# Kernel optimization log

Measured on AMD Instinct MI355X. Metric: run time of the kernel, lower is better.

The kernel has to match this reference:

```python
import jax, jax.numpy as jnp
import numpy as np

B, T, C, COND, H = 64, 4096, 64, 512, 256
SCALE_EPS = 1e-6
LOGSCALE_FACTOR = 3.0  # glow LinearZeros convention
LEAK = 0.01            # torch LeakyReLU default slope


def setup_inputs() -> dict:
    key = jax.random.key(0)
    ks = jax.random.split(key, 10)
    perm = jnp.asarray(np.random.RandomState(0).permutation(C), dtype=jnp.int32)
    return {
        "input_seq": jax.random.normal(ks[0], (B, T, C), jnp.float32),
        "speech_cond": jax.random.normal(ks[1], (B, T, COND), jnp.float32),
        "actnorm_bias": 0.1 * jax.random.normal(ks[2], (C,), jnp.float32),
        "actnorm_logs": 0.1 * jax.random.normal(ks[3], (C,), jnp.float32),
        "perm": perm,
        "W1": jax.random.normal(ks[4], (C // 2 + COND, H), jnp.float32) / np.sqrt(C // 2 + COND),
        "b1": 0.01 * jax.random.normal(ks[5], (H,), jnp.float32),
        "W2": 0.05 * jax.random.normal(ks[6], (H, C), jnp.float32) / np.sqrt(H),
        "b2": 0.01 * jax.random.normal(ks[7], (C,), jnp.float32),
        "logs2": 0.05 * jax.random.normal(ks[8], (C,), jnp.float32),
    }


def reference(input_seq, speech_cond, actnorm_bias, actnorm_logs, perm, W1, b1, W2, b2, logs2):
    # The torch module loops over timesteps, but each step is independent
    # (no RNN state is used), so we batch all timesteps at once.
    # --- ActNorm2d (per-channel affine); pixels=1 per timestep ---
    z = (input_seq + actnorm_bias) * jnp.exp(actnorm_logs)          # [B,T,C]
    logdet = jnp.full((B,), T * jnp.sum(actnorm_logs))              # [B]
    # --- Permute2d (fixed shuffle of channels) ---
    z = z[..., perm]
    # --- split coupling ---
    z1, z2 = z[..., : C // 2], z[..., C // 2 :]                     # [B,T,C/2] each
    # f_seq: Linear + LeakyReLU (dropout off at eval) + LinearZeros
    h = jnp.concatenate([z1, speech_cond], axis=-1)                 # [B,T,C/2+COND]
    h = jax.nn.leaky_relu(jnp.einsum("btk,kh->bth", h, W1) + b1, LEAK)
    h = (jnp.einsum("bth,hc->btc", h, W2) + b2) * jnp.exp(logs2 * LOGSCALE_FACTOR)  # [B,T,C]
    # --- affine transform: split 'cross' (interleaved) ---
    shift = h[..., 0::2]
    scale = jnp.maximum(jax.nn.sigmoid(h[..., 1::2] + 2.0), SCALE_EPS)
    z2 = (z2 + shift) * scale
    logdet = logdet + jnp.sum(jnp.log(scale), axis=(1, 2))          # [B]
    z_seq = jnp.concatenate([z1, z2], axis=-1)                      # [B,T,C]
    return z_seq, logdet
```

## Files before the change

kernel.cpp:

```cpp
#include <hip/hip_runtime.h>
#include <stdint.h>

#define B_ 64
#define T_ 4096
#define C_ 64
#define COND_ 512
#define H_ 256

typedef __attribute__((ext_vector_type(8))) short short8;
typedef __attribute__((ext_vector_type(4))) float f32x4;
typedef __attribute__((ext_vector_type(2))) float f32x2;
typedef __attribute__((ext_vector_type(2))) unsigned int u32x2;

__device__ __forceinline__ unsigned short f2bf(float x) {
  union { float f; unsigned u; } v; v.f = x;
  unsigned r = v.u + 0x7FFFu + ((v.u >> 16) & 1u);
  return (unsigned short)(r >> 16);
}

#define WS_W1   0
#define WS_W2   278528
#define WS_PB   311296
#define WS_PS   311552
#define WS_B2S  311808

__global__ __launch_bounds__(256) void prep_kernel(
    const float* __restrict__ W1, const float* __restrict__ W2,
    const float* __restrict__ anb, const float* __restrict__ anl,
    const int* __restrict__ perm, const float* __restrict__ b2,
    const float* __restrict__ logs2,
    unsigned short* __restrict__ wsW1, unsigned short* __restrict__ wsW2,
    float* __restrict__ pb, float* __restrict__ ps, float* __restrict__ b2s,
    float* __restrict__ out_ld)
{
  int id = blockIdx.x * 256 + threadIdx.x;
  if (id < 544 * 256) {
    int feat = id & 255, k = id >> 8;
    int r = (k < 512) ? (k + 32) : (k - 512);
    float v = W1[r * 256 + feat];
    int s = k >> 5, MI = feat >> 4;
    int l = (feat & 15) + 16 * ((k >> 3) & 3), i = k & 7;
    wsW1[((s * 16 + MI) * 64 + l) * 8 + i] = f2bf(v);
  } else if (id < 544 * 256 + 256 * 64) {
    int id2 = id - 544 * 256;
    int ch = id2 & 63, k = id2 >> 6;
    float v = W2[k * 64 + ch] * expf(logs2[ch] * 3.0f);
    int s2 = k >> 5, MI2 = ch >> 4;
    int l = (ch & 15) + 16 * ((k >> 3) & 3), i = k & 7;
    wsW2[((s2 * 4 + MI2) * 64 + l) * 8 + i] = f2bf(v);
  } else {
    int c = id - (544 * 256 + 256 * 64);
    if (c < 64) {
      int p = perm[c];
      pb[c] = anb[p];
      ps[c] = expf(anl[p]);
    } else if (c < 128) {
      int ch = c - 64;
      b2s[ch] = b2[ch] * expf(logs2[ch] * 3.0f);
    } else if (c < 192) {
      int b = c - 128;
      float s = 0.f;
      for (int j = 0; j < 64; ++j) s += anl[j];
      out_ld[b] = (float)T_ * s;
    }
  }
}

__global__ __launch_bounds__(256) void flow_main(
    const float* __restrict__ input, const float* __restrict__ cond,
    const int* __restrict__ perm, const float* __restrict__ b1,
    const unsigned short* __restrict__ wsW1, const unsigned short* __restrict__ wsW2,
    const float* __restrict__ pb, const float* __restrict__ ps,
    const float* __restrict__ b2s,
    float* __restrict__ out, float* __restrict__ out_ld)
{
  __shared__ short lA[2][64 * 64];
  __shared__ short lHT[64 * 256];

  const int tid = threadIdx.x;
  const int w  = tid >> 6;
  const int l  = tid & 63;
  const int lr = l & 15;
  const int lh = l >> 4;
  const long long m0 = (long long)blockIdx.x * 64;

  {
    const int tok = tid >> 2;
    const int c0 = (tid & 3) * 8;
    const float* ip = input + (m0 + tok) * 64;
    short8 v;
#pragma unroll
    for (int j = 0; j < 8; ++j) {
      int c = c0 + j;
      v[j] = (short)f2bf((ip[perm[c]] + pb[c]) * ps[c]);
    }
    const int S = (tid & 3) ^ (tok & 7);
    *(short8*)&lA[0][tok * 64 + S * 8] = v;
  }
  __syncthreads();

  f32x4 acc[4][4];
#pragma unroll
  for (int mi = 0; mi < 4; ++mi)
#pragma unroll
    for (int nj = 0; nj < 4; ++nj)
      acc[mi][nj] = (f32x4)0.0f;

  const int stok = tid >> 2;
  const int skc = (tid & 3) * 16;

#pragma unroll 1
  for (int it = 0; it <= 8; ++it) {
    const int buf = it & 1;

    f32x4 st0, st1, st2, st3;
    if (it < 8) {
      const float* cp = cond + (m0 + stok) * 512 + (it * 64 + skc);
      st0 = *(const f32x4*)(cp);
      st1 = *(const f32x4*)(cp + 4);
      st2 = *(const f32x4*)(cp + 8);
      st3 = *(const f32x4*)(cp + 12);
    }

    const int nk = (it == 0) ? 1 : 2;
    const int sbase = (it == 0) ? 16 : 2 * (it - 1);

    short8 af[2][4], bf[2][4];
#pragma unroll
    for (int h = 0; h < 2; ++h) {
      if (h < nk) {
#pragma unroll
        for (int mi = 0; mi < 4; ++mi)
          af[h][mi] = *(const short8*)&wsW1[(((sbase + h) * 16 + (4 * w + mi)) * 64 + l) * 8];
#pragma unroll
        for (int nj = 0; nj < 4; ++nj) {
          int tok = 16 * nj + lr;
          int S = (4 * h + lh) ^ (tok & 7);
          bf[h][nj] = *(const short8*)&lA[buf][tok * 64 + S * 8];
        }
      }
    }

#pragma unroll
    for (int h = 0; h < 2; ++h) {
      if (h < nk) {
#pragma unroll
        for (int mi = 0; mi < 4; ++mi)
#pragma unroll
          for (int nj = 0; nj < 4; ++nj)
            acc[mi][nj] = __builtin_amdgcn_mfma_f32_16x16x32_bf16(
                af[h][mi], bf[h][nj], acc[mi][nj], 0, 0, 0);
      }
    }

    if (it < 8) {
      short8 c0v, c1v;
      c0v[0] = (short)f2bf(st0[0]); c0v[1] = (short)f2bf(st0[1]);
      c0v[2] = (short)f2bf(st0[2]); c0v[3] = (short)f2bf(st0[3]);
      c0v[4] = (short)f2bf(st1[0]); c0v[5] = (short)f2bf(st1[1]);
      c0v[6] = (short)f2bf(st1[2]); c0v[7] = (short)f2bf(st1[3]);
      c1v[0] = (short)f2bf(st2[0]); c1v[1] = (short)f2bf(st2[1]);
      c1v[2] = (short)f2bf(st2[2]); c1v[3] = (short)f2bf(st2[3]);
      c1v[4] = (short)f2bf(st3[0]); c1v[5] = (short)f2bf(st3[1]);
      c1v[6] = (short)f2bf(st3[2]); c1v[7] = (short)f2bf(st3[3]);
      const int S0 = 2 * (tid & 3);
      *(short8*)&lA[buf ^ 1][stok * 64 + ((S0 ^ (stok & 7)) * 8)] = c0v;
      *(short8*)&lA[buf ^ 1][stok * 64 + (((S0 + 1) ^ (stok & 7)) * 8)] = c1v;
    }
    __syncthreads();
  }

#pragma unroll
  for (int mi = 0; mi < 4; ++mi) {
    const int f0 = 64 * w + 16 * mi + 4 * lh;
    const f32x4 b1v = *(const f32x4*)&b1[f0];
#pragma unroll
    for (int nj = 0; nj < 4; ++nj) {
      const int tok = 16 * nj + lr;
      f32x4 v = acc[mi][nj];
      float h0 = v[0] + b1v[0]; h0 = h0 > 0.f ? h0 : 0.01f * h0;
      float h1 = v[1] + b1v[1]; h1 = h1 > 0.f ? h1 : 0.01f * h1;
      float h2 = v[2] + b1v[2]; h2 = h2 > 0.f ? h2 : 0.01f * h2;
      float h3 = v[3] + b1v[3]; h3 = h3 > 0.f ? h3 : 0.01f * h3;
      u32x2 p;
      p[0] = (unsigned)f2bf(h0) | ((unsigned)f2bf(h1) << 16);
      p[1] = (unsigned)f2bf(h2) | ((unsigned)f2bf(h3) << 16);
      const int off = (tok * 512 + f0 * 2) ^ ((tok & 7) << 4);
      *(u32x2*)((char*)lHT + off) = p;
    }
  }
  __syncthreads();

  f32x4 acc2[4];
#pragma unroll
  for (int nj = 0; nj < 4; ++nj) acc2[nj] = (f32x4)0.0f;

#pragma unroll
  for (int s2 = 0; s2 < 8; ++s2) {
    const short8 a2 = *(const short8*)&wsW2[((s2 * 4 + w) * 64 + l) * 8];
#pragma unroll
    for (int nj = 0; nj < 4; ++nj) {
      const int tok = 16 * nj + lr;
      const int off = (tok * 512 + (32 * s2 + 8 * lh) * 2) ^ ((tok & 7) << 4);
      const short8 hb = *(const short8*)((char*)lHT + off);
      acc2[nj] = __builtin_amdgcn_mfma_f32_16x16x32_bf16(a2, hb, acc2[nj], 0, 0, 0);
    }
  }

  const int j0 = 8 * w + 2 * lh;
  const int pA = perm[j0],      pB = perm[j0 + 1];
  const int pC = perm[32 + j0], pD = perm[33 + j0];
  const float bA = pb[j0],      sA = ps[j0];
  const float bB = pb[j0 + 1],  sB = ps[j0 + 1];
  const float bC = pb[32 + j0], sC = ps[32 + j0];
  const float bD = pb[33 + j0], sD = ps[33 + j0];
  const f32x4 b2v = *(const f32x4*)&b2s[16 * w + 4 * lh];

  float ldp = 0.f;
#pragma unroll
  for (int nj = 0; nj < 4; ++nj) {
    const long long row = m0 + 16 * nj + lr;
    const float* ip = input + row * 64;
    float* op = out + row * 64;
    f32x4 v = acc2[nj];
    const float sh0 = v[0] + b2v[0];
    const float sc0 = v[1] + b2v[1];
    const float sh1 = v[2] + b2v[2];
    const float sc1 = v[3] + b2v[3];
    const float scl0 = fmaxf(1.f / (1.f + expf(-(sc0 + 2.f))), 1e-6f);
    const float scl1 = fmaxf(1.f / (1.f + expf(-(sc1 + 2.f))), 1e-6f);
    f32x2 z1o, z2o;
    z1o[0] = (ip[pA] + bA) * sA;
    z1o[1] = (ip[pB] + bB) * sB;
    z2o[0] = ((ip[pC] + bC) * sC + sh0) * scl0;
    z2o[1] = ((ip[pD] + bD) * sD + sh1) * scl1;
    *(f32x2*)(op + j0) = z1o;
    *(f32x2*)(op + 32 + j0) = z2o;
    ldp += logf(scl0) + logf(scl1);
  }

#pragma unroll
  for (int off = 32; off > 0; off >>= 1) ldp += __shfl_xor(ldp, off, 64);
  if (l == 0) atomicAdd(&out_ld[blockIdx.x >> 6], ldp);
}

extern "C" void kernel_launch(void* const* d_in, const int* in_sizes, int n_in,
                              void* d_out, int out_size, void* d_ws, size_t ws_size,
                              hipStream_t stream)
{
  const float* input = (const float*)d_in[0];
  const float* cond  = (const float*)d_in[1];
  const float* anb   = (const float*)d_in[2];
  const float* anl   = (const float*)d_in[3];
  const int*   perm  = (const int*)d_in[4];
  const float* W1    = (const float*)d_in[5];
  const float* b1    = (const float*)d_in[6];
  const float* W2    = (const float*)d_in[7];
  const float* b2    = (const float*)d_in[8];
  const float* logs2 = (const float*)d_in[9];

  float* out    = (float*)d_out;
  float* out_ld = out + (long long)B_ * T_ * C_;

  char* ws = (char*)d_ws;
  unsigned short* wsW1 = (unsigned short*)(ws + WS_W1);
  unsigned short* wsW2 = (unsigned short*)(ws + WS_W2);
  float* pbp  = (float*)(ws + WS_PB);
  float* psp  = (float*)(ws + WS_PS);
  float* b2sp = (float*)(ws + WS_B2S);

  prep_kernel<<<609, 256, 0, stream>>>(W1, W2, anb, anl, perm, b2, logs2,
                                       wsW1, wsW2, pbp, psp, b2sp, out_ld);
  flow_main<<<4096, 256, 0, stream>>>(input, cond, perm, b1, wsW1, wsW2,
                                      pbp, psp, b2sp, out, out_ld);
}
```

Measured before the change: 259.0 us.

## Load cond operands directly into registers, removing LDS staging and per-step barriers

```diff
diff --git a/kernel.cpp b/kernel.cpp
--- a/kernel.cpp
+++ b/kernel.cpp
@@ -74,7 +74,7 @@
     const float* __restrict__ b2s,
     float* __restrict__ out, float* __restrict__ out_ld)
 {
-  __shared__ short lA[2][64 * 64];
+  __shared__ short lA[64 * 64];
   __shared__ short lHT[64 * 256];
 
   const int tid = threadIdx.x;
@@ -95,9 +95,26 @@
       v[j] = (short)f2bf((ip[perm[c]] + pb[c]) * ps[c]);
     }
     const int S = (tid & 3) ^ (tok & 7);
-    *(short8*)&lA[0][tok * 64 + S * 8] = v;
-  }
-  __syncthreads();
+    *(short8*)&lA[tok * 64 + S * 8] = v;
+  }
+
+  const unsigned short* w1p = wsW1 + ((4 * w) * 64 + l) * 8;
+  const float* bbase = cond + (m0 + lr) * 512 + 8 * lh;
+
+  short8 aZ[4], aC[4];
+  f32x4 bst[8];
+#pragma unroll
+  for (int mi = 0; mi < 4; ++mi)
+    aZ[mi] = *(const short8*)&w1p[16 * 8192 + mi * 512];
+#pragma unroll
+  for (int mi = 0; mi < 4; ++mi)
+    aC[mi] = *(const short8*)&w1p[0 * 8192 + mi * 512];
+#pragma unroll
+  for (int nj = 0; nj < 4; ++nj) {
+    const float* p = bbase + nj * 8192;
+    bst[2 * nj]     = *(const f32x4*)p;
+    bst[2 * nj + 1] = *(const f32x4*)(p + 4);
+  }
 
   f32x4 acc[4][4];
 #pragma unroll
@@ -106,68 +123,65 @@
     for (int nj = 0; nj < 4; ++nj)
       acc[mi][nj] = (f32x4)0.0f;
 
-  const int stok = tid >> 2;
-  const int skc = (tid & 3) * 16;
+  __syncthreads();
+
+  {
+    short8 bz[4];
+#pragma unroll
+    for (int nj = 0; nj < 4; ++nj) {
+      const int tok = 16 * nj + lr;
+      const int S = lh ^ (tok & 7);
+      bz[nj] = *(const short8*)&lA[tok * 64 + S * 8];
+    }
+#pragma unroll
+    for (int mi = 0; mi < 4; ++mi)
+#pragma unroll
+      for (int nj = 0; nj < 4; ++nj)
+        acc[mi][nj] = __builtin_amdgcn_mfma_f32_16x16x32_bf16(
+            aZ[mi], bz[nj], acc[mi][nj], 0, 0, 0);
+  }
 
 #pragma unroll 1
-  for (int it = 0; it <= 8; ++it) {
-    const int buf = it & 1;
-
-    f32x4 st0, st1, st2, st3;
-    if (it < 8) {
-      const float* cp = cond + (m0 + stok) * 512 + (it * 64 + skc);
-      st0 = *(const f32x4*)(cp);
-      st1 = *(const f32x4*)(cp + 4);
-      st2 = *(const f32x4*)(cp + 8);
-      st3 = *(const f32x4*)(cp + 12);
-    }
-
-    const int nk = (it == 0) ? 1 : 2;
-    const int sbase = (it == 0) ? 16 : 2 * (it - 1);
-
-    short8 af[2][4], bf[2][4];
-#pragma unroll
-    for (int h = 0; h < 2; ++h) {
-      if (h < nk) {
-#pragma unroll
-        for (int mi = 0; mi < 4; ++mi)
-          af[h][mi] = *(const short8*)&wsW1[(((sbase + h) * 16 + (4 * w + mi)) * 64 + l) * 8];
-#pragma unroll
-        for (int nj = 0; nj < 4; ++nj) {
-          int tok = 16 * nj + lr;
-          int S = (4 * h + lh) ^ (tok & 7);
-          bf[h][nj] = *(const short8*)&lA[buf][tok * 64 + S * 8];
-        }
+  for (int q = 0; q < 16; ++q) {
+    short8 aN[4];
+    if (q < 15) {
+#pragma unroll
+      for (int mi = 0; mi < 4; ++mi)
+        aN[mi] = *(const short8*)&w1p[(q + 1) * 8192 + mi * 512];
+    }
+
+    short8 bfr[4];
+#pragma unroll
+    for (int nj = 0; nj < 4; ++nj) {
+      const f32x4 lo = bst[2 * nj], hi = bst[2 * nj + 1];
+      short8 t;
+      t[0] = (short)f2bf(lo[0]); t[1] = (short)f2bf(lo[1]);
+      t[2] = (short)f2bf(lo[2]); t[3] = (short)f2bf(lo[3]);
+      t[4] = (short)f2bf(hi[0]); t[5] = (short)f2bf(hi[1]);
+      t[6] = (short)f2bf(hi[2]); t[7] = (short)f2bf(hi[3]);
+      bfr[nj] = t;
+    }
+
+    if (q < 15) {
+#pragma unroll
+      for (int nj = 0; nj < 4; ++nj) {
+        const float* p = bbase + nj * 8192 + (q + 1) * 32;
+        bst[2 * nj]     = *(const f32x4*)p;
+        bst[2 * nj + 1] = *(const f32x4*)(p + 4);
       }
     }
 
 #pragma unroll
-    for (int h = 0; h < 2; ++h) {
-      if (h < nk) {
-#pragma unroll
-        for (int mi = 0; mi < 4; ++mi)
-#pragma unroll
-          for (int nj = 0; nj < 4; ++nj)
-            acc[mi][nj] = __builtin_amdgcn_mfma_f32_16x16x32_bf16(
-                af[h][mi], bf[h][nj], acc[mi][nj], 0, 0, 0);
-      }
-    }
-
-    if (it < 8) {
-      short8 c0v, c1v;
-      c0v[0] = (short)f2bf(st0[0]); c0v[1] = (short)f2bf(st0[1]);
-      c0v[2] = (short)f2bf(st0[2]); c0v[3] = (short)f2bf(st0[3]);
-      c0v[4] = (short)f2bf(st1[0]); c0v[5] = (short)f2bf(st1[1]);
-      c0v[6] = (short)f2bf(st1[2]); c0v[7] = (short)f2bf(st1[3]);
-      c1v[0] = (short)f2bf(st2[0]); c1v[1] = (short)f2bf(st2[1]);
-      c1v[2] = (short)f2bf(st2[2]); c1v[3] = (short)f2bf(st2[3]);
-      c1v[4] = (short)f2bf(st3[0]); c1v[5] = (short)f2bf(st3[1]);
-      c1v[6] = (short)f2bf(st3[2]); c1v[7] = (short)f2bf(st3[3]);
-      const int S0 = 2 * (tid & 3);
-      *(short8*)&lA[buf ^ 1][stok * 64 + ((S0 ^ (stok & 7)) * 8)] = c0v;
-      *(short8*)&lA[buf ^ 1][stok * 64 + (((S0 + 1) ^ (stok & 7)) * 8)] = c1v;
-    }
-    __syncthreads();
+    for (int mi = 0; mi < 4; ++mi)
+#pragma unroll
+      for (int nj = 0; nj < 4; ++nj)
+        acc[mi][nj] = __builtin_amdgcn_mfma_f32_16x16x32_bf16(
+            aC[mi], bfr[nj], acc[mi][nj], 0, 0, 0);
+
+    if (q < 15) {
+#pragma unroll
+      for (int mi = 0; mi < 4; ++mi) aC[mi] = aN[mi];
+    }
   }
 
 #pragma unroll
@@ -189,6 +203,12 @@
       *(u32x2*)((char*)lHT + off) = p;
     }
   }
+
+  short8 a2r[8];
+#pragma unroll
+  for (int s2 = 0; s2 < 8; ++s2)
+    a2r[s2] = *(const short8*)&wsW2[((s2 * 4 + w) * 64 + l) * 8];
+
   __syncthreads();
 
   f32x4 acc2[4];
@@ -197,13 +217,12 @@
 
 #pragma unroll
   for (int s2 = 0; s2 < 8; ++s2) {
-    const short8 a2 = *(const short8*)&wsW2[((s2 * 4 + w) * 64 + l) * 8];
 #pragma unroll
     for (int nj = 0; nj < 4; ++nj) {
       const int tok = 16 * nj + lr;
       const int off = (tok * 512 + (32 * s2 + 8 * lh) * 2) ^ ((tok & 7) << 4);
       const short8 hb = *(const short8*)((char*)lHT + off);
-      acc2[nj] = __builtin_amdgcn_mfma_f32_16x16x32_bf16(a2, hb, acc2[nj], 0, 0, 0);
+      acc2[nj] = __builtin_amdgcn_mfma_f32_16x16x32_bf16(a2r[s2], hb, acc2[nj], 0, 0, 0);
     }
   }
 
```

Result: slower. 379.5 us (+46.5%).
